# Optimization experiments

Measured on AMD Instinct MI355X. Metric: run time of the kernel, lower is better.

Reference implementation:

```python
import jax, jax.numpy as jnp
import numpy as np
from jax import lax


def _conv(x, w):
    # 3x3 conv, stride 1, SAME padding, NCHW/OIHW layout, no bias
    return lax.conv_general_dilated(
        x, w, window_strides=(1, 1), padding='SAME',
        dimension_numbers=('NCHW', 'OIHW', 'NCHW'))


def _interleave2x2(tl, tr, bl, br):
    # each [B,H,W] -> [B,2H,2W] with tl at (0::2,0::2), tr at (0::2,1::2), etc.
    top = jnp.stack([tl, tr], axis=-1)          # [B,H,W,2]
    bot = jnp.stack([bl, br], axis=-1)          # [B,H,W,2]
    x = jnp.stack([top, bot], axis=2)           # [B,H,2,W,2]
    B, H, _, W, _ = x.shape
    return x.reshape(B, 2 * H, 2 * W)


def setup_inputs() -> dict:
    key = jax.random.key(0)
    ks = jax.random.split(key, 8)
    B, H, W = 16, 512, 512
    width = 12
    s = 0.1  # weight scale, approximates xavier for tiny fan-ins
    return {
        'mosaic': jax.random.normal(ks[0], (B, 4, H, W), jnp.float32),
        'fw0': jax.random.normal(ks[1], (width, 4, 3, 3), jnp.float32) * s,
        'fw1': jax.random.normal(ks[2], (width, width, 3, 3), jnp.float32) * s,
        'fw2': jax.random.normal(ks[3], (width, width, 3, 3), jnp.float32) * s,
        'ww0': jax.random.normal(ks[4], (width, 4, 3, 3), jnp.float32) * s,
        'ww1': jax.random.normal(ks[5], (width, width, 3, 3), jnp.float32) * s,
        'ww2': jax.random.normal(ks[6], (width, width, 3, 3), jnp.float32) * s,
        'cw0': jax.random.normal(ks[7], (6, 2, 3, 3), jnp.float32) * s,
    }


def reference(mosaic, fw0, fw1, fw2, ww0, ww1, ww2, cw0):
    width = fw0.shape[0]  # 12
    half = width // 2

    f = jax.nn.relu(_conv(mosaic, fw0))
    f = jax.nn.relu(_conv(f, fw1))
    interps = jax.nn.relu(_conv(f, fw2))

    w = jax.nn.relu(_conv(mosaic, ww0))
    w = jax.nn.relu(_conv(w, ww1))
    w = jax.nn.relu(_conv(w, ww2))
    weights = jax.nn.softmax(w, axis=1)

    mul = interps * weights                              # [B,12,H,W]
    # green_rb[:,0] = sum of first half, green_rb[:,1] = sum of second half
    green_rb = jnp.stack(
        [mul[:, :half].sum(axis=1), mul[:, half:].sum(axis=1)], axis=1)  # [B,2,H,W]

    # green_add channels: [mosaic0, g1, mosaic3, mosaic0, g0, mosaic3]
    green_add = jnp.stack([
        mosaic[:, 0], green_rb[:, 1], mosaic[:, 3],
        mosaic[:, 0], green_rb[:, 0], mosaic[:, 3]], axis=1)  # [B,6,H,W]

    # chroma: (rb - green_rb) -> single conv 2->6 (chroma_depth=1, no relu)
    rb = jnp.stack([mosaic[:, 1], mosaic[:, 2]], axis=1)  # [B,2,H,W]
    chroma_diff = _conv(rb - green_rb, cw0)               # [B,6,H,W]
    chroma_pred = chroma_diff + green_add

    # pixel-shuffle assembly of full-res RGB [B,3,2H,2W]
    r = _interleave2x2(chroma_pred[:, 0], mosaic[:, 1], chroma_pred[:, 1], chroma_pred[:, 2])
    g = _interleave2x2(mosaic[:, 0], green_rb[:, 0], green_rb[:, 1], mosaic[:, 3])
    b = _interleave2x2(chroma_pred[:, 3], chroma_pred[:, 4], mosaic[:, 2], chroma_pred[:, 5])
    return jnp.stack([r, g, b], axis=1)
```

## Files before the change

kernel.cpp:

```cpp
#include <hip/hip_runtime.h>
#include <cstdint>

#define HH 512
#define WW 512
#define TX 58

typedef __attribute__((ext_vector_type(8)))  short    short8;
typedef __attribute__((ext_vector_type(16))) float    f32x16;
typedef __attribute__((ext_vector_type(2)))  unsigned u32x2;
typedef long long lng;

union FragU { uint4 u; short8 s; };
union U4L   { uint4 u; lng l[2]; };
union B8U   { u32x2 u2[2]; short8 s; };
union BL    { unsigned w[2]; lng l; };

#define L1F_O  0
#define L1W_O  8928
#define L1RST  744
#define MOS_O  17856
#define MOSR   512
#define L2F_O  17856
#define L2W_O  25056
#define L2RST  720
#define RELAY_O 0
#define SMEMB  32256

__device__ __forceinline__ unsigned cvtpk(float a, float b) {
  unsigned r;
  asm("v_cvt_pk_bf16_f32 %0, %1, %2" : "=v"(r) : "v"(a), "v"(b));
  return r;
}
__device__ __forceinline__ unsigned rpk8(float a, float b, float c, float d, bool im) {
  int r = __builtin_amdgcn_cvt_pk_fp8_f32(fmaxf(a, 0.f), fmaxf(b, 0.f), 0, false);
  r = __builtin_amdgcn_cvt_pk_fp8_f32(fmaxf(c, 0.f), fmaxf(d, 0.f), r, true);
  return im ? (unsigned)r : 0u;
}
__device__ __forceinline__ unsigned short f2bf(float f) {
  union { float f; unsigned u; } v; v.f = f;
  unsigned r = v.u + 0x7fffu + ((v.u >> 16) & 1u);
  return (unsigned short)(r >> 16);
}
__device__ __forceinline__ float bf2f(unsigned short b) {
  union { unsigned u; float f; } v; v.u = ((unsigned)b) << 16;
  return v.f;
}
__device__ __forceinline__ float lo16(unsigned u) {
  union { unsigned v; float f; } x; x.v = u << 16; return x.f;
}
__device__ __forceinline__ float hi16(unsigned u) {
  union { unsigned v; float f; } x; x.v = u & 0xffff0000u; return x.f;
}
__device__ __forceinline__ lng rd8(const char* p) {
  BL t;
  t.w[0] = *(const unsigned*)p;
  t.w[1] = *(const unsigned*)(p + 4);
  return t.l;
}

__global__ void wt_kernel(const float* __restrict__ fw0, const float* __restrict__ fw1,
                          const float* __restrict__ fw2, const float* __restrict__ ww0,
                          const float* __restrict__ ww1, const float* __restrict__ ww2,
                          uint4* __restrict__ wsf) {
  int t = blockIdx.x * 256 + threadIdx.x;
  if (t >= 31 * 64) return;
  int f = t >> 6, lane = t & 63;
  int h = (lane >> 5) & 1, m = lane & 31;
  uint4 o = make_uint4(0, 0, 0, 0);
  if (f < 3) {
    unsigned short v[8];
#pragma unroll
    for (int e = 0; e < 8; ++e) {
      int sq = 2 * h + (e >> 2);
      int c4 = e & 3;
      float w = 0.f;
      if (sq < 3 && m < 24) {
        w = (m < 12) ? fw0[(m * 4 + c4) * 9 + f * 3 + sq]
                     : ww0[((m - 12) * 4 + c4) * 9 + f * 3 + sq];
      }
      v[e] = f2bf(w);
    }
    o.x = (unsigned)v[0] | ((unsigned)v[1] << 16);
    o.y = (unsigned)v[2] | ((unsigned)v[3] << 16);
    o.z = (unsigned)v[4] | ((unsigned)v[5] << 16);
    o.w = (unsigned)v[6] | ((unsigned)v[7] << 16);
  } else {
    const int PR[7][2][2] = {
      {{0, 1}, {2, 3}}, {{4, 5}, {6, 7}}, {{9, 10}, {11, 12}},
      {{13, 14}, {15, 16}}, {{18, 19}, {20, 21}}, {{22, 23}, {24, 25}},
      {{8, 17}, {26, -1}}};
    int fi = f - 3, layer = fi / 14, path = (fi % 14) / 7, j = fi % 7;
    const float* src = layer ? (path ? ww2 : fw2) : (path ? ww1 : fw1);
    const float scale = (layer == 1 && path == 1) ? 1.44269504f : 1.0f;
    float wv[8];
#pragma unroll
    for (int p = 0; p < 8; ++p) {
      int q = PR[j][h][p >> 2];
      int c = p & 3;
      float w = 0.f;
      if (q >= 0 && m < 12) {
        int kap = 4 * q + c;
        int tap = kap / 12, ci = kap % 12;
        w = src[(m * 12 + ci) * 9 + tap] * scale;
      }
      wv[p] = w;
    }
    int x = __builtin_amdgcn_cvt_pk_fp8_f32(wv[0], wv[1], 0, false);
    x = __builtin_amdgcn_cvt_pk_fp8_f32(wv[2], wv[3], x, true);
    int y = __builtin_amdgcn_cvt_pk_fp8_f32(wv[4], wv[5], 0, false);
    y = __builtin_amdgcn_cvt_pk_fp8_f32(wv[6], wv[7], y, true);
    o.x = (unsigned)x; o.y = (unsigned)y;
  }
  wsf[t] = o;
}

template<int RST, int WIN>
__device__ __forceinline__ void conv12f8(const lng* aF, const lng* aW,
                                         const char* Ph, const char* Pa, const char* Pb,
                                         int imm, f32x16& cF, f32x16& cW) {
  const int IM[6] = {0, 16, RST, RST + 16, 2 * RST, 2 * RST + 16};
#pragma unroll
  for (int j = 0; j < 6; ++j) {
    lng bF = rd8(Ph + imm + IM[j]);
    lng bW = rd8(Ph + imm + IM[j] + WIN);
    cF = __builtin_amdgcn_mfma_f32_32x32x16_fp8_fp8(aF[j], bF, cF, 0, 0, 0);
    cW = __builtin_amdgcn_mfma_f32_32x32x16_fp8_fp8(aW[j], bW, cW, 0, 0, 0);
  }
  {
    BL bF, bW;
    bF.w[0] = *(const unsigned*)(Pa + imm + 32);
    bF.w[1] = *(const unsigned*)(Pb + imm + 32);
    bW.w[0] = *(const unsigned*)(Pa + imm + 32 + WIN);
    bW.w[1] = *(const unsigned*)(Pb + imm + 32 + WIN);
    cF = __builtin_amdgcn_mfma_f32_32x32x16_fp8_fp8(aF[6], bF.l, cF, 0, 0, 0);
    cW = __builtin_amdgcn_mfma_f32_32x32x16_fp8_fp8(aW[6], bW.l, cW, 0, 0, 0);
  }
}

template<int WOUT>
__device__ __forceinline__ void store12f8(char* pO, int imm, const f32x16& cF,
                                          const f32x16& cW, bool im, int h) {
  *(unsigned*)(pO + imm) = rpk8(cF[0], cF[1], cF[2], cF[3], im);
  *(unsigned*)(pO + imm + WOUT) = rpk8(cW[0], cW[1], cW[2], cW[3], im);
  if (h == 0) {
    *(unsigned*)(pO + imm + 8) = rpk8(cF[4], cF[5], cF[6], cF[7], im);
    *(unsigned*)(pO + imm + WOUT + 8) = rpk8(cW[4], cW[5], cW[6], cW[7], im);
  }
}

__global__ __launch_bounds__(256, 5)
void green_kernel(const float* __restrict__ mosaic, const uint4* __restrict__ wsf,
                  unsigned short* __restrict__ green) {
  __shared__ __align__(16) char s[SMEMB];
  const int tid = threadIdx.x;
  const int lane = tid & 63;
  const int wv = __builtin_amdgcn_readfirstlane(tid >> 6);
  const int h = (lane >> 5) & 1, ln = lane & 31;
  const int ln8 = ln * 8, ln12 = ln * 12;
  const int bid = blockIdx.x;
  const int bx = bid % 9;
  const int t9 = bid / 9;
  const int by = t9 & 63, b = t9 >> 6;
  const int X0 = bx * TX, Y0 = by * 8;

  {
    const float* mb = mosaic + (size_t)b * 4 * HH * WW;
    for (int p = tid; p < 14 * 64; p += 256) {
      int row = p >> 6, col = p & 63;
      int gy = Y0 + row - 3, gx = X0 + col - 3;
      float c0 = 0.f, c1 = 0.f, c2 = 0.f, c3 = 0.f;
      if ((unsigned)gy < HH && (unsigned)gx < WW) {
        const float* mp = mb + (size_t)gy * WW + gx;
        c0 = mp[0]; c1 = mp[HH * WW]; c2 = mp[2 * HH * WW]; c3 = mp[3 * HH * WW];
      }
      u32x2 w = { cvtpk(c0, c1), cvtpk(c2, c3) };
      *(u32x2*)(s + MOS_O + row * MOSR + col * 8) = w;
    }
  }
  __syncthreads();

  {
    FragU a3[3];
#pragma unroll
    for (int q = 0; q < 3; ++q) a3[q].u = wsf[q * 64 + lane];
    const char* pLo = s + MOS_O + 3 * wv * MOSR + ln8 + 16 * h;
    const char* pHi = s + MOS_O + 3 * wv * MOSR + ln8 + 8;
    char* base = s + 3 * wv * L1RST + ln12;
    char* pA = base + L1F_O + 4 * h;
    char* pB = h ? base + L1W_O : base + L1F_O + 8;
    char* pC = base + L1W_O + (h ? 8 : 4);
    bool ck[2];
    ck[0] = (unsigned)(X0 + 0  + ln - 2) < WW;
    ck[1] = (unsigned)(X0 + 30 + ln - 2) < WW;
#pragma unroll
    for (int r = 0; r < 3; ++r) {
      const int ly = 3 * wv + r;
      const bool rowok = (unsigned)(Y0 + ly - 2) < HH;
#pragma unroll
      for (int g = 0; g < 2; ++g) {
        const int cb = g * 30;
        f32x16 c = {};
#pragma unroll
        for (int ky = 0; ky < 3; ++ky) {
          B8U bu;
          bu.u2[0] = *(const u32x2*)(pLo + (r + ky) * MOSR + cb * 8);
          bu.u2[1] = *(const u32x2*)(pHi + (r + ky) * MOSR + cb * 8);
          c = __builtin_amdgcn_mfma_f32_32x32x16_bf16(a3[ky].s, bu.s, c, 0, 0, 0);
        }
        const bool im = rowok && ck[g];
        *(unsigned*)(pA + r * L1RST + cb * 12) = rpk8(c[0], c[1], c[2], c[3], im);
        *(unsigned*)(pB + r * L1RST + cb * 12) = rpk8(c[4], c[5], c[6], c[7], im);
        *(unsigned*)(pC + r * L1RST + cb * 12) = rpk8(c[8], c[9], c[10], c[11], im);
      }
    }
  }
  __syncthreads();

  {
    lng aF[7], aW[7];
#pragma unroll
    for (int j = 0; j < 7; ++j) {
      U4L u; u.u = wsf[(3 + j) * 64 + lane];  aF[j] = u.l[0];
      U4L v; v.u = wsf[(10 + j) * 64 + lane]; aW[j] = v.l[0];
    }
    const char* base = s + L1F_O + wv * L1RST + ln12;
    const char* Ph = base + 8 * h;
    const char* Pa = base + (h ? 2 * L1RST : 0);
    const char* Pb = base + (h ? 2 * L1RST : L1RST);
    char* bO0 = s + L2F_O + wv * L2RST + ln12 + 4 * h;
    bool ck[2];
    ck[0] = (unsigned)(X0 + 0  + ln - 1) < WW;
    ck[1] = (unsigned)(X0 + 28 + ln - 1) < WW;
#pragma unroll
    for (int i = 0; i < 3; ++i) {
      const int ly = wv + 4 * i;
      if (ly < 10) {
        const bool rowok = (unsigned)(Y0 + ly - 1) < HH;
#pragma unroll
        for (int g = 0; g < 2; ++g) {
          const int cb = g * 28;
          f32x16 cF = {}, cW = {};
          conv12f8<L1RST, 8928>(aF, aW, Ph, Pa, Pb, i * 4 * L1RST + cb * 12, cF, cW);
          store12f8<7200>(bO0, i * 4 * L2RST + cb * 12, cF, cW, rowok && ck[g], h);
        }
      }
    }
  }
  __syncthreads();

  {
    lng aF[7], aW[7];
#pragma unroll
    for (int j = 0; j < 7; ++j) {
      U4L u; u.u = wsf[(17 + j) * 64 + lane]; aF[j] = u.l[0];
      U4L v; v.u = wsf[(24 + j) * 64 + lane]; aW[j] = v.l[0];
    }
    const char* base = s + L2F_O + 2 * wv * L2RST + ln12;
    const char* Ph = base + 8 * h;
    const char* Pa = base + (h ? 2 * L2RST : 0);
    const char* Pb = base + (h ? 2 * L2RST : L2RST);
    char* slot = s + RELAY_O + (wv * 32 + ln) * 48;
#pragma unroll
    for (int r = 0; r < 2; ++r) {
#pragma unroll
      for (int g = 0; g < 2; ++g) {
        const int cb = g * 26;
        f32x16 cF = {}, cW = {};
        conv12f8<L2RST, 7200>(aF, aW, Ph, Pa, Pb, r * L2RST + cb * 12, cF, cW);
        const int cidx = g & 1;
        if (cidx == 0) {
          if (h) {
            uint4 pay;
            pay.x = cvtpk(fmaxf(cF[0], 0.f), fmaxf(cF[1], 0.f));
            pay.y = cvtpk(fmaxf(cF[2], 0.f), fmaxf(cF[3], 0.f));
            pay.z = cvtpk(fmaxf(cW[0], 0.f), fmaxf(cW[1], 0.f));
            pay.w = cvtpk(fmaxf(cW[2], 0.f), fmaxf(cW[3], 0.f));
            *(uint4*)slot = pay;
          }
        } else {
          if (!h) {
            uint4 pa, pb;
            pa.x = cvtpk(fmaxf(cF[0], 0.f), fmaxf(cF[1], 0.f));
            pa.y = cvtpk(fmaxf(cF[2], 0.f), fmaxf(cF[3], 0.f));
            pa.z = cvtpk(fmaxf(cF[4], 0.f), fmaxf(cF[5], 0.f));
            pa.w = cvtpk(fmaxf(cF[6], 0.f), fmaxf(cF[7], 0.f));
            pb.x = cvtpk(fmaxf(cW[0], 0.f), fmaxf(cW[1], 0.f));
            pb.y = cvtpk(fmaxf(cW[2], 0.f), fmaxf(cW[3], 0.f));
            pb.z = cvtpk(fmaxf(cW[4], 0.f), fmaxf(cW[5], 0.f));
            pb.w = cvtpk(fmaxf(cW[6], 0.f), fmaxf(cW[7], 0.f));
            *(uint4*)slot = pa;
            *(uint4*)(slot + 16) = pb;
          }
        }
        asm volatile("s_waitcnt lgkmcnt(0)" ::: "memory");
        if (h == cidx) {
          float F[12], Wv[12];
          if (cidx == 0) {
            const uint4 pay = *(const uint4*)slot;
#pragma unroll
            for (int c2 = 0; c2 < 4; ++c2) {
              F[c2]      = fmaxf(cF[c2], 0.f);
              F[8 + c2]  = fmaxf(cF[4 + c2], 0.f);
              Wv[c2]     = fmaxf(cW[c2], 0.f);
              Wv[8 + c2] = fmaxf(cW[4 + c2], 0.f);
            }
            F[4] = lo16(pay.x);  F[5] = hi16(pay.x);
            F[6] = lo16(pay.y);  F[7] = hi16(pay.y);
            Wv[4] = lo16(pay.z); Wv[5] = hi16(pay.z);
            Wv[6] = lo16(pay.w); Wv[7] = hi16(pay.w);
          } else {
            const uint4 pa = *(const uint4*)slot;
            const uint4 pb = *(const uint4*)(slot + 16);
#pragma unroll
            for (int c2 = 0; c2 < 4; ++c2) {
              F[4 + c2]  = fmaxf(cF[c2], 0.f);
              Wv[4 + c2] = fmaxf(cW[c2], 0.f);
            }
            F[0] = lo16(pa.x);   F[1] = hi16(pa.x);
            F[2] = lo16(pa.y);   F[3] = hi16(pa.y);
            F[8] = lo16(pa.z);   F[9] = hi16(pa.z);
            F[10] = lo16(pa.w);  F[11] = hi16(pa.w);
            Wv[0] = lo16(pb.x);  Wv[1] = hi16(pb.x);
            Wv[2] = lo16(pb.y);  Wv[3] = hi16(pb.y);
            Wv[8] = lo16(pb.z);  Wv[9] = hi16(pb.z);
            Wv[10] = lo16(pb.w); Wv[11] = hi16(pb.w);
          }
          float m = 0.f;
#pragma unroll
          for (int c2 = 0; c2 < 12; ++c2) m = fmaxf(m, Wv[c2]);
          float sum = 0.f, s0 = 0.f, s1 = 0.f;
#pragma unroll
          for (int c2 = 0; c2 < 12; ++c2) {
            const float e = exp2f(Wv[c2] - m);
            sum += e;
            if (c2 < 6) s0 = fmaf(F[c2], e, s0);
            else        s1 = fmaf(F[c2], e, s1);
          }
          const float inv = 1.f / sum;
          const unsigned pg = cvtpk(s0 * inv, s1 * inv);
          const int gy = Y0 + 2 * wv + r;
          const int gx = X0 + cb + ln;
          if ((unsigned)gx < WW) {
            green[((b * 2 + 0) * HH + gy) * WW + gx] = (unsigned short)pg;
            green[((b * 2 + 1) * HH + gy) * WW + gx] = (unsigned short)(pg >> 16);
          }
        }
      }
    }
  }
}

__global__ __launch_bounds__(256)
void assemble_kernel(const float* __restrict__ mosaic, const unsigned short* __restrict__ green,
                     const float* __restrict__ cw0, float* __restrict__ out) {
  const int t = blockIdx.x * 256 + threadIdx.x;
  const int x = t & (WW - 1);
  const int y = (t >> 9) & (HH - 1);
  const int b = t >> 18;

  const int p = y * WW + x;
  const float* __restrict__ mb = mosaic + (size_t)b * 4 * HH * WW;
  const unsigned short* __restrict__ gb = green + (size_t)b * 2 * HH * WW;

  const float m0 = mb[p];
  const float m1 = mb[HH * WW + p];
  const float m2 = mb[2 * HH * WW + p];
  const float m3 = mb[3 * HH * WW + p];
  const float g0 = bf2f(gb[p]);
  const float g1 = bf2f(gb[HH * WW + p]);

  float cd[6] = {0.f, 0.f, 0.f, 0.f, 0.f, 0.f};
#pragma unroll
  for (int ky = 0; ky < 3; ++ky) {
#pragma unroll
    for (int kx = 0; kx < 3; ++kx) {
      const int yy = y + ky - 1, xx = x + kx - 1;
      float c0 = 0.f, c1 = 0.f;
      if ((unsigned)yy < HH && (unsigned)xx < WW) {
        const int q = yy * WW + xx;
        c0 = mb[HH * WW + q]     - bf2f(gb[q]);
        c1 = mb[2 * HH * WW + q] - bf2f(gb[HH * WW + q]);
      }
      const int k = ky * 3 + kx;
#pragma unroll
      for (int o = 0; o < 6; ++o) {
        cd[o] = fmaf(c0, cw0[(o * 2 + 0) * 9 + k], cd[o]);
        cd[o] = fmaf(c1, cw0[(o * 2 + 1) * 9 + k], cd[o]);
      }
    }
  }
  const float cp0 = cd[0] + m0;
  const float cp1 = cd[1] + g1;
  const float cp2 = cd[2] + m3;
  const float cp3 = cd[3] + m0;
  const float cp4 = cd[4] + g0;
  const float cp5 = cd[5] + m3;

  const int W2 = 2 * WW;
  const size_t plane = (size_t)(2 * HH) * W2;
  size_t base = ((size_t)(b * 3) * (2 * HH) + 2 * y) * W2 + 2 * x;
  *(float2*)(out + base)              = make_float2(cp0, m1);
  *(float2*)(out + base + W2)         = make_float2(cp1, cp2);
  *(float2*)(out + base + plane)      = make_float2(m0, g0);
  *(float2*)(out + base + plane + W2) = make_float2(g1, m3);
  *(float2*)(out + base + 2 * plane)      = make_float2(cp3, cp4);
  *(float2*)(out + base + 2 * plane + W2) = make_float2(m2, cp5);
}

extern "C" void kernel_launch(void* const* d_in, const int* in_sizes, int n_in,
                              void* d_out, int out_size, void* d_ws, size_t ws_size,
                              hipStream_t stream) {
  const float* mosaic = (const float*)d_in[0];
  const float* fw0 = (const float*)d_in[1];
  const float* fw1 = (const float*)d_in[2];
  const float* fw2 = (const float*)d_in[3];
  const float* ww0 = (const float*)d_in[4];
  const float* ww1 = (const float*)d_in[5];
  const float* ww2 = (const float*)d_in[6];
  const float* cw0 = (const float*)d_in[7];

  uint4* wsf = (uint4*)((char*)d_ws + 32768);
  unsigned short* green = (unsigned short*)((char*)d_ws + 67584);
  float* out = (float*)d_out;

  wt_kernel<<<8, 256, 0, stream>>>(fw0, fw1, fw2, ww0, ww1, ww2, wsf);
  green_kernel<<<16 * 64 * 9, 256, 0, stream>>>(mosaic, wsf, green);
  assemble_kernel<<<(16 * HH * WW) / 256, 256, 0, stream>>>(mosaic, green, cw0, out);
}
```

Measured before the change: 225.5 us.

## Use 16x16x128 scaled FP8 MFMA for the 12-channel conv layers

Replaces the seven chained 32x32x16 FP8 MFMAs per output tile in conv layers 2 and 3 with one 16x16x128 scaled FP8 MFMA (unit scales) per 16-pixel row, and repacks the weights into the new K=108-padded-to-128 fragment layout. Each wave now covers a fixed 16-column strip over all rows, and the softmax relay is reorganised so every lane holds one full pixel's 12 channels. The aim is fewer MFMA issues and less accumulator overhead, at the cost of about 16% wasted K and more LDS gather loads per fragment. It also changes the wave-to-pixel mapping, so the last wave's strip overlaps the others.

```diff
diff --git a/kernel.cpp b/kernel.cpp
--- a/kernel.cpp
+++ b/kernel.cpp
@@ -7,13 +7,14 @@
 
 typedef __attribute__((ext_vector_type(8)))  short    short8;
 typedef __attribute__((ext_vector_type(16))) float    f32x16;
+typedef __attribute__((ext_vector_type(4)))  float    f32x4;
 typedef __attribute__((ext_vector_type(2)))  unsigned u32x2;
-typedef long long lng;
+typedef __attribute__((ext_vector_type(8)))  int      int8v;
 
 union FragU { uint4 u; short8 s; };
-union U4L   { uint4 u; lng l[2]; };
 union B8U   { u32x2 u2[2]; short8 s; };
-union BL    { unsigned w[2]; lng l; };
+union AF8   { uint4 u[2]; int8v v; };
+union BF8   { unsigned d[8]; int8v v; };
 
 #define L1F_O  0
 #define L1W_O  8928
@@ -24,7 +25,10 @@
 #define L2W_O  25056
 #define L2RST  720
 #define RELAY_O 0
-#define SMEMB  32256
+#define SMEMB  32320
+
+#define MFMA_SC(A, B, C) \
+  __builtin_amdgcn_mfma_scale_f32_16x16x128_f8f6f4((A), (B), (C), 0, 0, 0, 0x7F7F7F7Fu, 0, 0x7F7F7F7Fu)
 
 __device__ __forceinline__ unsigned cvtpk(float a, float b) {
   unsigned r;
@@ -50,12 +54,6 @@
 }
 __device__ __forceinline__ float hi16(unsigned u) {
   union { unsigned v; float f; } x; x.v = u & 0xffff0000u; return x.f;
-}
-__device__ __forceinline__ lng rd8(const char* p) {
-  BL t;
-  t.w[0] = *(const unsigned*)p;
-  t.w[1] = *(const unsigned*)(p + 4);
-  return t.l;
 }
 
 __global__ void wt_kernel(const float* __restrict__ fw0, const float* __restrict__ fw1,
@@ -63,11 +61,10 @@
                           const float* __restrict__ ww1, const float* __restrict__ ww2,
                           uint4* __restrict__ wsf) {
   int t = blockIdx.x * 256 + threadIdx.x;
-  if (t >= 31 * 64) return;
-  int f = t >> 6, lane = t & 63;
-  int h = (lane >> 5) & 1, m = lane & 31;
-  uint4 o = make_uint4(0, 0, 0, 0);
-  if (f < 3) {
+  if (t >= 448) return;
+  if (t < 192) {
+    int f = t >> 6, lane = t & 63;
+    int h = (lane >> 5) & 1, m = lane & 31;
     unsigned short v[8];
 #pragma unroll
     for (int e = 0; e < 8; ++e) {
@@ -80,71 +77,47 @@
       }
       v[e] = f2bf(w);
     }
+    uint4 o;
     o.x = (unsigned)v[0] | ((unsigned)v[1] << 16);
     o.y = (unsigned)v[2] | ((unsigned)v[3] << 16);
     o.z = (unsigned)v[4] | ((unsigned)v[5] << 16);
     o.w = (unsigned)v[6] | ((unsigned)v[7] << 16);
+    wsf[t] = o;
   } else {
-    const int PR[7][2][2] = {
-      {{0, 1}, {2, 3}}, {{4, 5}, {6, 7}}, {{9, 10}, {11, 12}},
-      {{13, 14}, {15, 16}}, {{18, 19}, {20, 21}}, {{22, 23}, {24, 25}},
-      {{8, 17}, {26, -1}}};
-    int fi = f - 3, layer = fi / 14, path = (fi % 14) / 7, j = fi % 7;
+    int u = t - 192, sid = u >> 6, lane = u & 63;
+    int m = lane & 15, kg = lane >> 4;
+    int layer = sid >> 1, path = sid & 1;
     const float* src = layer ? (path ? ww2 : fw2) : (path ? ww1 : fw1);
     const float scale = (layer == 1 && path == 1) ? 1.44269504f : 1.0f;
-    float wv[8];
-#pragma unroll
-    for (int p = 0; p < 8; ++p) {
-      int q = PR[j][h][p >> 2];
-      int c = p & 3;
-      float w = 0.f;
-      if (q >= 0 && m < 12) {
-        int kap = 4 * q + c;
-        int tap = kap / 12, ci = kap % 12;
-        w = src[(m * 12 + ci) * 9 + tap] * scale;
-      }
-      wv[p] = w;
-    }
-    int x = __builtin_amdgcn_cvt_pk_fp8_f32(wv[0], wv[1], 0, false);
-    x = __builtin_amdgcn_cvt_pk_fp8_f32(wv[2], wv[3], x, true);
-    int y = __builtin_amdgcn_cvt_pk_fp8_f32(wv[4], wv[5], 0, false);
-    y = __builtin_amdgcn_cvt_pk_fp8_f32(wv[6], wv[7], y, true);
-    o.x = (unsigned)x; o.y = (unsigned)y;
-  }
-  wsf[t] = o;
-}
-
-template<int RST, int WIN>
-__device__ __forceinline__ void conv12f8(const lng* aF, const lng* aW,
-                                         const char* Ph, const char* Pa, const char* Pb,
-                                         int imm, f32x16& cF, f32x16& cW) {
-  const int IM[6] = {0, 16, RST, RST + 16, 2 * RST, 2 * RST + 16};
-#pragma unroll
-  for (int j = 0; j < 6; ++j) {
-    lng bF = rd8(Ph + imm + IM[j]);
-    lng bW = rd8(Ph + imm + IM[j] + WIN);
-    cF = __builtin_amdgcn_mfma_f32_32x32x16_fp8_fp8(aF[j], bF, cF, 0, 0, 0);
-    cW = __builtin_amdgcn_mfma_f32_32x32x16_fp8_fp8(aW[j], bW, cW, 0, 0, 0);
-  }
-  {
-    BL bF, bW;
-    bF.w[0] = *(const unsigned*)(Pa + imm + 32);
-    bF.w[1] = *(const unsigned*)(Pb + imm + 32);
-    bW.w[0] = *(const unsigned*)(Pa + imm + 32 + WIN);
-    bW.w[1] = *(const unsigned*)(Pb + imm + 32 + WIN);
-    cF = __builtin_amdgcn_mfma_f32_32x32x16_fp8_fp8(aF[6], bF.l, cF, 0, 0, 0);
-    cW = __builtin_amdgcn_mfma_f32_32x32x16_fp8_fp8(aW[6], bW.l, cW, 0, 0, 0);
-  }
-}
-
-template<int WOUT>
-__device__ __forceinline__ void store12f8(char* pO, int imm, const f32x16& cF,
-                                          const f32x16& cW, bool im, int h) {
-  *(unsigned*)(pO + imm) = rpk8(cF[0], cF[1], cF[2], cF[3], im);
-  *(unsigned*)(pO + imm + WOUT) = rpk8(cW[0], cW[1], cW[2], cW[3], im);
-  if (h == 0) {
-    *(unsigned*)(pO + imm + 8) = rpk8(cF[4], cF[5], cF[6], cF[7], im);
-    *(unsigned*)(pO + imm + WOUT + 8) = rpk8(cW[4], cW[5], cW[6], cW[7], im);
+    unsigned d[8];
+#pragma unroll
+    for (int k = 0; k < 8; ++k) {
+      float w4[4];
+#pragma unroll
+      for (int j4 = 0; j4 < 4; ++j4) {
+        int e = 4 * k + j4;
+        float w = 0.f;
+        if (m < 12) {
+          if (kg < 3) {
+            int dx = e / 12, ci = e % 12, tap = kg * 3 + dx;
+            w = src[(m * 12 + ci) * 9 + tap] * scale;
+          } else {
+            int i = e >> 3, j = e & 7;
+            if (i < 3 && j < 4) {
+              int tap = i * 3 + 2, ci = 8 + j;
+              w = src[(m * 12 + ci) * 9 + tap] * scale;
+            }
+          }
+        }
+        w4[j4] = w;
+      }
+      int x = __builtin_amdgcn_cvt_pk_fp8_f32(w4[0], w4[1], 0, false);
+      x = __builtin_amdgcn_cvt_pk_fp8_f32(w4[2], w4[3], x, true);
+      d[k] = (unsigned)x;
+    }
+    uint4* dst = wsf + 192 + sid * 128 + lane * 2;
+    dst[0] = make_uint4(d[0], d[1], d[2], d[3]);
+    dst[1] = make_uint4(d[4], d[5], d[6], d[7]);
   }
 }
 
@@ -157,6 +130,7 @@
   const int wv = __builtin_amdgcn_readfirstlane(tid >> 6);
   const int h = (lane >> 5) & 1, ln = lane & 31;
   const int ln8 = ln * 8, ln12 = ln * 12;
+  const int pxl = lane & 15, kg = lane >> 4;
   const int bid = blockIdx.x;
   const int bx = bid % 9;
   const int t9 = bid / 9;
@@ -217,135 +191,120 @@
   __syncthreads();
 
   {
-    lng aF[7], aW[7];
-#pragma unroll
-    for (int j = 0; j < 7; ++j) {
-      U4L u; u.u = wsf[(3 + j) * 64 + lane];  aF[j] = u.l[0];
-      U4L v; v.u = wsf[(10 + j) * 64 + lane]; aW[j] = v.l[0];
-    }
-    const char* base = s + L1F_O + wv * L1RST + ln12;
-    const char* Ph = base + 8 * h;
-    const char* Pa = base + (h ? 2 * L1RST : 0);
-    const char* Pb = base + (h ? 2 * L1RST : L1RST);
-    char* bO0 = s + L2F_O + wv * L2RST + ln12 + 4 * h;
-    bool ck[2];
-    ck[0] = (unsigned)(X0 + 0  + ln - 1) < WW;
-    ck[1] = (unsigned)(X0 + 28 + ln - 1) < WW;
-#pragma unroll
-    for (int i = 0; i < 3; ++i) {
-      const int ly = wv + 4 * i;
-      if (ly < 10) {
-        const bool rowok = (unsigned)(Y0 + ly - 1) < HH;
-#pragma unroll
-        for (int g = 0; g < 2; ++g) {
-          const int cb = g * 28;
-          f32x16 cF = {}, cW = {};
-          conv12f8<L1RST, 8928>(aF, aW, Ph, Pa, Pb, i * 4 * L1RST + cb * 12, cF, cW);
-          store12f8<7200>(bO0, i * 4 * L2RST + cb * 12, cF, cW, rowok && ck[g], h);
-        }
+    AF8 aF, aW;
+    aF.u[0] = wsf[192 + lane * 2]; aF.u[1] = wsf[193 + lane * 2];
+    aW.u[0] = wsf[320 + lane * 2]; aW.u[1] = wsf[321 + lane * 2];
+    const int c0 = (wv == 0) ? 0 : (wv == 1) ? 16 : (wv == 2) ? 32 : 44;
+    int o0, o1, o2, o3;
+    if (kg < 3) { o0 = kg * L1RST + pxl * 12; o1 = o0 + 8; o2 = o0 + 16; o3 = o0 + 24; }
+    else        { o0 = (pxl + 2) * 12 + 8; o1 = o0 + L1RST; o2 = o1 + L1RST; o3 = o2; }
+    const char* P0 = s + L1F_O + c0 * 12 + o0;
+    const char* P1 = s + L1F_O + c0 * 12 + o1;
+    const char* P2 = s + L1F_O + c0 * 12 + o2;
+    const char* P3 = s + L1F_O + c0 * 12 + o3;
+    const bool ckx = (unsigned)(X0 + c0 + pxl - 1) < WW;
+    char* pO = s + L2F_O + (c0 + pxl) * 12 + 4 * kg;
+#pragma unroll
+    for (int ly = 0; ly < 10; ++ly) {
+      const int imm = ly * L1RST;
+      BF8 bF, bW;
+      bF.d[0] = *(const unsigned*)(P0 + imm);        bF.d[1] = *(const unsigned*)(P0 + imm + 4);
+      bF.d[2] = *(const unsigned*)(P1 + imm);        bF.d[3] = *(const unsigned*)(P1 + imm + 4);
+      bF.d[4] = *(const unsigned*)(P2 + imm);        bF.d[5] = *(const unsigned*)(P2 + imm + 4);
+      bF.d[6] = *(const unsigned*)(P3 + imm);        bF.d[7] = *(const unsigned*)(P3 + imm + 4);
+      bW.d[0] = *(const unsigned*)(P0 + imm + 8928); bW.d[1] = *(const unsigned*)(P0 + imm + 8932);
+      bW.d[2] = *(const unsigned*)(P1 + imm + 8928); bW.d[3] = *(const unsigned*)(P1 + imm + 8932);
+      bW.d[4] = *(const unsigned*)(P2 + imm + 8928); bW.d[5] = *(const unsigned*)(P2 + imm + 8932);
+      bW.d[6] = *(const unsigned*)(P3 + imm + 8928); bW.d[7] = *(const unsigned*)(P3 + imm + 8932);
+      f32x4 cF = {0.f, 0.f, 0.f, 0.f}, cW = {0.f, 0.f, 0.f, 0.f};
+      cF = MFMA_SC(aF.v, bF.v, cF);
+      cW = MFMA_SC(aW.v, bW.v, cW);
+      const bool im = ckx && ((unsigned)(Y0 + ly - 1) < HH);
+      if (kg < 3) {
+        *(unsigned*)(pO + ly * L2RST)        = rpk8(cF[0], cF[1], cF[2], cF[3], im);
+        *(unsigned*)(pO + ly * L2RST + 7200) = rpk8(cW[0], cW[1], cW[2], cW[3], im);
       }
     }
   }
   __syncthreads();
 
   {
-    lng aF[7], aW[7];
-#pragma unroll
-    for (int j = 0; j < 7; ++j) {
-      U4L u; u.u = wsf[(17 + j) * 64 + lane]; aF[j] = u.l[0];
-      U4L v; v.u = wsf[(24 + j) * 64 + lane]; aW[j] = v.l[0];
-    }
-    const char* base = s + L2F_O + 2 * wv * L2RST + ln12;
-    const char* Ph = base + 8 * h;
-    const char* Pa = base + (h ? 2 * L2RST : 0);
-    const char* Pb = base + (h ? 2 * L2RST : L2RST);
-    char* slot = s + RELAY_O + (wv * 32 + ln) * 48;
-#pragma unroll
-    for (int r = 0; r < 2; ++r) {
-#pragma unroll
-      for (int g = 0; g < 2; ++g) {
-        const int cb = g * 26;
-        f32x16 cF = {}, cW = {};
-        conv12f8<L2RST, 7200>(aF, aW, Ph, Pa, Pb, r * L2RST + cb * 12, cF, cW);
-        const int cidx = g & 1;
-        if (cidx == 0) {
-          if (h) {
-            uint4 pay;
-            pay.x = cvtpk(fmaxf(cF[0], 0.f), fmaxf(cF[1], 0.f));
-            pay.y = cvtpk(fmaxf(cF[2], 0.f), fmaxf(cF[3], 0.f));
-            pay.z = cvtpk(fmaxf(cW[0], 0.f), fmaxf(cW[1], 0.f));
-            pay.w = cvtpk(fmaxf(cW[2], 0.f), fmaxf(cW[3], 0.f));
-            *(uint4*)slot = pay;
-          }
-        } else {
-          if (!h) {
-            uint4 pa, pb;
-            pa.x = cvtpk(fmaxf(cF[0], 0.f), fmaxf(cF[1], 0.f));
-            pa.y = cvtpk(fmaxf(cF[2], 0.f), fmaxf(cF[3], 0.f));
-            pa.z = cvtpk(fmaxf(cF[4], 0.f), fmaxf(cF[5], 0.f));
-            pa.w = cvtpk(fmaxf(cF[6], 0.f), fmaxf(cF[7], 0.f));
-            pb.x = cvtpk(fmaxf(cW[0], 0.f), fmaxf(cW[1], 0.f));
-            pb.y = cvtpk(fmaxf(cW[2], 0.f), fmaxf(cW[3], 0.f));
-            pb.z = cvtpk(fmaxf(cW[4], 0.f), fmaxf(cW[5], 0.f));
-            pb.w = cvtpk(fmaxf(cW[6], 0.f), fmaxf(cW[7], 0.f));
-            *(uint4*)slot = pa;
-            *(uint4*)(slot + 16) = pb;
-          }
-        }
-        asm volatile("s_waitcnt lgkmcnt(0)" ::: "memory");
-        if (h == cidx) {
-          float F[12], Wv[12];
-          if (cidx == 0) {
-            const uint4 pay = *(const uint4*)slot;
-#pragma unroll
-            for (int c2 = 0; c2 < 4; ++c2) {
-              F[c2]      = fmaxf(cF[c2], 0.f);
-              F[8 + c2]  = fmaxf(cF[4 + c2], 0.f);
-              Wv[c2]     = fmaxf(cW[c2], 0.f);
-              Wv[8 + c2] = fmaxf(cW[4 + c2], 0.f);
-            }
-            F[4] = lo16(pay.x);  F[5] = hi16(pay.x);
-            F[6] = lo16(pay.y);  F[7] = hi16(pay.y);
-            Wv[4] = lo16(pay.z); Wv[5] = hi16(pay.z);
-            Wv[6] = lo16(pay.w); Wv[7] = hi16(pay.w);
-          } else {
-            const uint4 pa = *(const uint4*)slot;
-            const uint4 pb = *(const uint4*)(slot + 16);
-#pragma unroll
-            for (int c2 = 0; c2 < 4; ++c2) {
-              F[4 + c2]  = fmaxf(cF[c2], 0.f);
-              Wv[4 + c2] = fmaxf(cW[c2], 0.f);
-            }
-            F[0] = lo16(pa.x);   F[1] = hi16(pa.x);
-            F[2] = lo16(pa.y);   F[3] = hi16(pa.y);
-            F[8] = lo16(pa.z);   F[9] = hi16(pa.z);
-            F[10] = lo16(pa.w);  F[11] = hi16(pa.w);
-            Wv[0] = lo16(pb.x);  Wv[1] = hi16(pb.x);
-            Wv[2] = lo16(pb.y);  Wv[3] = hi16(pb.y);
-            Wv[8] = lo16(pb.z);  Wv[9] = hi16(pb.z);
-            Wv[10] = lo16(pb.w); Wv[11] = hi16(pb.w);
-          }
-          float m = 0.f;
-#pragma unroll
-          for (int c2 = 0; c2 < 12; ++c2) m = fmaxf(m, Wv[c2]);
-          float sum = 0.f, s0 = 0.f, s1 = 0.f;
-#pragma unroll
-          for (int c2 = 0; c2 < 12; ++c2) {
-            const float e = exp2f(Wv[c2] - m);
-            sum += e;
-            if (c2 < 6) s0 = fmaf(F[c2], e, s0);
-            else        s1 = fmaf(F[c2], e, s1);
-          }
-          const float inv = 1.f / sum;
-          const unsigned pg = cvtpk(s0 * inv, s1 * inv);
-          const int gy = Y0 + 2 * wv + r;
-          const int gx = X0 + cb + ln;
-          if ((unsigned)gx < WW) {
-            green[((b * 2 + 0) * HH + gy) * WW + gx] = (unsigned short)pg;
-            green[((b * 2 + 1) * HH + gy) * WW + gx] = (unsigned short)(pg >> 16);
-          }
-        }
-      }
+    AF8 aF, aW;
+    aF.u[0] = wsf[448 + lane * 2]; aF.u[1] = wsf[449 + lane * 2];
+    aW.u[0] = wsf[576 + lane * 2]; aW.u[1] = wsf[577 + lane * 2];
+    const int c0 = (wv == 0) ? 0 : (wv == 1) ? 16 : (wv == 2) ? 32 : 42;
+    int o0, o1, o2, o3;
+    if (kg < 3) { o0 = kg * L2RST + pxl * 12; o1 = o0 + 8; o2 = o0 + 16; o3 = o0 + 24; }
+    else        { o0 = (pxl + 2) * 12 + 8; o1 = o0 + L2RST; o2 = o1 + L2RST; o3 = o2; }
+    const char* P0 = s + L2F_O + c0 * 12 + o0;
+    const char* P1 = s + L2F_O + c0 * 12 + o1;
+    const char* P2 = s + L2F_O + c0 * 12 + o2;
+    const char* P3 = s + L2F_O + c0 * 12 + o3;
+    char* relay = s + RELAY_O + wv * 3072;
+#pragma unroll
+    for (int half = 0; half < 2; ++half) {
+#pragma unroll
+      for (int rr = 0; rr < 4; ++rr) {
+        const int imm = (half * 4 + rr) * L2RST;
+        BF8 bF, bW;
+        bF.d[0] = *(const unsigned*)(P0 + imm);        bF.d[1] = *(const unsigned*)(P0 + imm + 4);
+        bF.d[2] = *(const unsigned*)(P1 + imm);        bF.d[3] = *(const unsigned*)(P1 + imm + 4);
+        bF.d[4] = *(const unsigned*)(P2 + imm);        bF.d[5] = *(const unsigned*)(P2 + imm + 4);
+        bF.d[6] = *(const unsigned*)(P3 + imm);        bF.d[7] = *(const unsigned*)(P3 + imm + 4);
+        bW.d[0] = *(const unsigned*)(P0 + imm + 7200); bW.d[1] = *(const unsigned*)(P0 + imm + 7204);
+        bW.d[2] = *(const unsigned*)(P1 + imm + 7200); bW.d[3] = *(const unsigned*)(P1 + imm + 7204);
+        bW.d[4] = *(const unsigned*)(P2 + imm + 7200); bW.d[5] = *(const unsigned*)(P2 + imm + 7204);
+        bW.d[6] = *(const unsigned*)(P3 + imm + 7200); bW.d[7] = *(const unsigned*)(P3 + imm + 7204);
+        f32x4 cF = {0.f, 0.f, 0.f, 0.f}, cW = {0.f, 0.f, 0.f, 0.f};
+        cF = MFMA_SC(aF.v, bF.v, cF);
+        cW = MFMA_SC(aW.v, bW.v, cW);
+        if (kg < 3) {
+          char* slot = relay + ((rr << 4) + pxl) * 48 + kg * 8;
+          u32x2 fv = { cvtpk(fmaxf(cF[0], 0.f), fmaxf(cF[1], 0.f)),
+                       cvtpk(fmaxf(cF[2], 0.f), fmaxf(cF[3], 0.f)) };
+          u32x2 wvv = { cvtpk(fmaxf(cW[0], 0.f), fmaxf(cW[1], 0.f)),
+                        cvtpk(fmaxf(cW[2], 0.f), fmaxf(cW[3], 0.f)) };
+          *(u32x2*)slot = fv;
+          *(u32x2*)(slot + 24) = wvv;
+        }
+      }
+      asm volatile("s_waitcnt lgkmcnt(0)" ::: "memory");
+      {
+        const char* slot = relay + lane * 48;
+        u32x2 f0 = *(const u32x2*)(slot);
+        u32x2 f1 = *(const u32x2*)(slot + 8);
+        u32x2 f2 = *(const u32x2*)(slot + 16);
+        u32x2 w0 = *(const u32x2*)(slot + 24);
+        u32x2 w1 = *(const u32x2*)(slot + 32);
+        u32x2 w2 = *(const u32x2*)(slot + 40);
+        float F[12], Wv[12];
+        F[0] = lo16(f0.x);  F[1] = hi16(f0.x);  F[2] = lo16(f0.y);  F[3] = hi16(f0.y);
+        F[4] = lo16(f1.x);  F[5] = hi16(f1.x);  F[6] = lo16(f1.y);  F[7] = hi16(f1.y);
+        F[8] = lo16(f2.x);  F[9] = hi16(f2.x);  F[10] = lo16(f2.y); F[11] = hi16(f2.y);
+        Wv[0] = lo16(w0.x); Wv[1] = hi16(w0.x); Wv[2] = lo16(w0.y); Wv[3] = hi16(w0.y);
+        Wv[4] = lo16(w1.x); Wv[5] = hi16(w1.x); Wv[6] = lo16(w1.y); Wv[7] = hi16(w1.y);
+        Wv[8] = lo16(w2.x); Wv[9] = hi16(w2.x); Wv[10] = lo16(w2.y); Wv[11] = hi16(w2.y);
+        float m = 0.f;
+#pragma unroll
+        for (int c2 = 0; c2 < 12; ++c2) m = fmaxf(m, Wv[c2]);
+        float sum = 0.f, s0 = 0.f, s1 = 0.f;
+#pragma unroll
+        for (int c2 = 0; c2 < 12; ++c2) {
+          const float e = exp2f(Wv[c2] - m);
+          sum += e;
+          if (c2 < 6) s0 = fmaf(F[c2], e, s0);
+          else        s1 = fmaf(F[c2], e, s1);
+        }
+        const float inv = 1.f / sum;
+        const unsigned pg = cvtpk(s0 * inv, s1 * inv);
+        const int gy = Y0 + half * 4 + kg;
+        const int gx = X0 + c0 + pxl;
+        if ((unsigned)gx < WW) {
+          green[((b * 2 + 0) * HH + gy) * WW + gx] = (unsigned short)pg;
+          green[((b * 2 + 1) * HH + gy) * WW + gx] = (unsigned short)(pg >> 16);
+        }
+      }
+      asm volatile("s_waitcnt lgkmcnt(0)" ::: "memory");
     }
   }
 }
@@ -423,7 +382,7 @@
   unsigned short* green = (unsigned short*)((char*)d_ws + 67584);
   float* out = (float*)d_out;
 
-  wt_kernel<<<8, 256, 0, stream>>>(fw0, fw1, fw2, ww0, ww1, ww2, wsf);
+  wt_kernel<<<2, 256, 0, stream>>>(fw0, fw1, fw2, ww0, ww1, ww2, wsf);
   green_kernel<<<16 * 64 * 9, 256, 0, stream>>>(mosaic, wsf, green);
   assemble_kernel<<<(16 * HH * WW) / 256, 256, 0, stream>>>(mosaic, green, cw0, out);
 }
```

Result: faster. 202.6 us (-10.1%).
